# Performance work log

Hardware: AMD Instinct MI355X
Metric: run time of the kernel (lower is better)

## Reference

```python
import jax, jax.numpy as jnp
import numpy as np

D_MODEL = 1024
N_HEADS = 16
D_HEAD = D_MODEL // N_HEADS
D_FF = 4096
THETA = 10000.0
EPS = 1e-5


def rmsnorm(x, g):
    xf = x.astype(jnp.float32)
    rms = jnp.sqrt(jnp.mean(xf * xf, axis=-1, keepdims=True) + EPS)
    return ((xf / rms) * g).astype(x.dtype)


def rope(x, pos):
    # x: (B, H, S, d_head); pos: (S,) int
    dk = x.shape[-1]
    inv_freq = 1.0 / (THETA ** (jnp.arange(0, dk, 2, dtype=jnp.float32) / dk))
    freqs = pos.astype(jnp.float32)[:, None] * inv_freq[None, :]  # (S, dk/2)
    cos, sin = jnp.cos(freqs), jnp.sin(freqs)
    xp = x.reshape(*x.shape[:-1], dk // 2, 2)
    xe, xo = xp[..., 0], xp[..., 1]
    re = xe * cos - xo * sin
    ro = xe * sin + xo * cos
    return jnp.stack([re, ro], axis=-1).reshape(x.shape)


def attention(x, pos, q_w, k_w, v_w, o_w):
    B, S, D = x.shape
    def heads(t):
        return t.reshape(B, S, N_HEADS, D_HEAD).transpose(0, 2, 1, 3)
    Q = heads(x @ q_w.T)
    K = heads(x @ k_w.T)
    V = heads(x @ v_w.T)
    Q = rope(Q, pos)
    K = rope(K, pos)
    scores = jnp.einsum('bhqd,bhkd->bhqk', Q, K) / jnp.sqrt(jnp.float32(D_HEAD))
    causal = jnp.tril(jnp.ones((S, S), dtype=bool))
    scores = jnp.where(causal[None, None], scores, -jnp.inf)
    attn = jax.nn.softmax(scores, axis=-1)
    H = jnp.einsum('bhqk,bhkd->bhqd', attn, V)
    H = H.transpose(0, 2, 1, 3).reshape(B, S, D)
    return H @ o_w.T


def swiglu(x, w1, w2, w3):
    a = x @ w1.T
    swish = a * jax.nn.sigmoid(a)
    gate = x @ w3.T
    return (swish * gate) @ w2.T


def setup_inputs() -> dict:
    key = jax.random.key(0)
    ks = jax.random.split(key, 8)
    B, S = 4, 2048
    std_ff = (2.0 / (D_MODEL + D_FF)) ** 0.5
    return {
        'x': jax.random.normal(ks[0], (B, S, D_MODEL), jnp.float32),
        'token_positions': jnp.arange(S, dtype=jnp.int32),
        'q_w': jax.random.truncated_normal(ks[1], -3, 3, (D_MODEL, D_MODEL), jnp.float32),
        'k_w': jax.random.truncated_normal(ks[2], -3, 3, (D_MODEL, D_MODEL), jnp.float32),
        'v_w': jax.random.truncated_normal(ks[3], -3, 3, (D_MODEL, D_MODEL), jnp.float32),
        'o_w': jax.random.truncated_normal(ks[4], -3, 3, (D_MODEL, D_MODEL), jnp.float32),
        'g1': jnp.ones((D_MODEL,), jnp.float32),
        'g2': jnp.ones((D_MODEL,), jnp.float32),
        'w1': jax.random.truncated_normal(ks[5], -3, 3, (D_FF, D_MODEL), jnp.float32) * std_ff,
        'w2': jax.random.truncated_normal(ks[6], -3, 3, (D_MODEL, D_FF), jnp.float32) * std_ff,
        'w3': jax.random.truncated_normal(ks[7], -3, 3, (D_FF, D_MODEL), jnp.float32) * std_ff,
    }


def reference(x, token_positions, q_w, k_w, v_w, o_w, g1, g2, w1, w2, w3):
    x_norm = rmsnorm(x, g1)
    O = x + attention(x_norm, token_positions, q_w, k_w, v_w, o_w)
    H = O + swiglu(rmsnorm(O, g2), w1, w2, w3)
    return H
```

## Files before the change

### kernel.cpp

```cpp
#include <hip/hip_runtime.h>
#include <stdint.h>


typedef short bf16x8 __attribute__((ext_vector_type(8)));
typedef float f32x4  __attribute__((ext_vector_type(4)));

#define DEV static __device__ __forceinline__

DEV float bf2f(uint32_t u) { uint32_t v = u << 16; float f; __builtin_memcpy(&f, &v, 4); return f; }
DEV uint16_t f2bf(float f) {
  uint32_t u; __builtin_memcpy(&u, &f, 4);
  u = (u + 0x7fffu + ((u >> 16) & 1u)) >> 16;
  return (uint16_t)u;
}

DEV void gl_lds16(const uint16_t* g, uint16_t* l) {
  __builtin_amdgcn_global_load_lds((const __attribute__((address_space(1))) uint32_t*)g,
                                   (__attribute__((address_space(3))) uint32_t*)l, 16, 0, 0);
}


__global__ __launch_bounds__(256) void cvt_bf16_k(const float* __restrict__ src,
                                                  uint16_t* __restrict__ dst, int n4) {
  const int t = blockIdx.x * 256 + threadIdx.x;
  if (t >= n4) return;
  const float4 v = ((const float4*)src)[t];
  ushort4 o; o.x = f2bf(v.x); o.y = f2bf(v.y); o.z = f2bf(v.z); o.w = f2bf(v.w);
  ((ushort4*)dst)[t] = o;
}

__global__ __launch_bounds__(256) void cvt_split_qk_k(const float* __restrict__ qw,
                                                      const float* __restrict__ kw,
                                                      uint16_t* __restrict__ hi,
                                                      uint16_t* __restrict__ lo) {
  const int t = blockIdx.x * 256 + threadIdx.x;
  const int row = t >> 8, c4 = t & 255;
  const float* src = (row < 1024) ? (qw + (size_t)row * 1024)
                                  : (kw + (size_t)(row - 1024) * 1024);
  const float4 v = ((const float4*)src)[c4];
  ushort4 h, l;
  h.x = f2bf(v.x); l.x = f2bf(v.x - bf2f(h.x));
  h.y = f2bf(v.y); l.y = f2bf(v.y - bf2f(h.y));
  h.z = f2bf(v.z); l.z = f2bf(v.z - bf2f(h.z));
  h.w = f2bf(v.w); l.w = f2bf(v.w - bf2f(h.w));
  ((ushort4*)hi)[t] = h; ((ushort4*)lo)[t] = l;
}


template <bool SPLIT>
__global__ __launch_bounds__(256) void rmsnorm_k(const float* __restrict__ xin,
                                                 const float* __restrict__ g,
                                                 uint16_t* __restrict__ hi,
                                                 uint16_t* __restrict__ lo) {
  const int row = blockIdx.x, t = threadIdx.x;
  const float4 v = ((const float4*)(xin + (size_t)row * 1024))[t];
  float ss = v.x * v.x + v.y * v.y + v.z * v.z + v.w * v.w;
#pragma unroll
  for (int m = 1; m < 64; m <<= 1) ss += __shfl_xor(ss, m);
  __shared__ float red[4];
  if ((t & 63) == 0) red[t >> 6] = ss;
  __syncthreads();
  const float rinv = rsqrtf((red[0] + red[1] + red[2] + red[3]) * (1.0f / 1024.0f) + 1e-5f);
  const float4 gv = ((const float4*)g)[t];
  float y[4] = { v.x * rinv * gv.x, v.y * rinv * gv.y, v.z * rinv * gv.z, v.w * rinv * gv.w };
  ushort4 h; h.x = f2bf(y[0]); h.y = f2bf(y[1]); h.z = f2bf(y[2]); h.w = f2bf(y[3]);
  ((ushort4*)(hi + (size_t)row * 1024))[t] = h;
  if constexpr (SPLIT) {
    ushort4 l;
    l.x = f2bf(y[0] - bf2f(h.x)); l.y = f2bf(y[1] - bf2f(h.y));
    l.z = f2bf(y[2] - bf2f(h.z)); l.w = f2bf(y[3] - bf2f(h.w));
    ((ushort4*)(lo + (size_t)row * 1024))[t] = l;
  }
}


template <int OUT>
__global__ __launch_bounds__(256) void gemm_bt_k(const uint16_t* __restrict__ A,
                                                 const uint16_t* __restrict__ B,
                                                 void* __restrict__ C,
                                                 const float* __restrict__ resid,
                                                 int N, int K) {
  __shared__ __align__(16) uint16_t As[128 * 64];
  __shared__ __align__(16) uint16_t Bs[128 * 64];
  const int t = threadIdx.x, w = t >> 6, lane = t & 63, m16 = lane & 15, quad = lane >> 4;
  const int wm = (w >> 1) * 64, wn = (w & 1) * 64;
  const int mBase = blockIdx.y * 128, nBase = blockIdx.x * 128;
  f32x4 acc[4][4];
  const f32x4 vz = {0.f, 0.f, 0.f, 0.f};
#pragma unroll
  for (int i = 0; i < 4; ++i)
#pragma unroll
    for (int j = 0; j < 4; ++j) acc[i][j] = vz;
  const int r_ = t >> 3, g_ = t & 7, sg = g_ ^ (r_ & 7);
  const uint16_t* ag = A + (size_t)(mBase + r_) * K + sg * 8;
  const uint16_t* bg = B + (size_t)(nBase + r_) * K + sg * 8;
  for (int k0 = 0; k0 < K; k0 += 64) {
#pragma unroll
    for (int it = 0; it < 4; ++it) {
      gl_lds16(ag + (size_t)(it * 32) * K + k0, As + it * 2048 + t * 8);
      gl_lds16(bg + (size_t)(it * 32) * K + k0, Bs + it * 2048 + t * 8);
    }
    __syncthreads();
#pragma unroll
    for (int ks = 0; ks < 2; ++ks) {
      bf16x8 af[4], bf4[4];
      const int cg = ks * 4 + quad;
#pragma unroll
      for (int i = 0; i < 4; ++i) {
        const int rA = wm + i * 16 + m16;
        af[i] = *(const bf16x8*)(As + rA * 64 + ((cg ^ (rA & 7)) * 8));
        const int rB = wn + i * 16 + m16;
        bf4[i] = *(const bf16x8*)(Bs + rB * 64 + ((cg ^ (rB & 7)) * 8));
      }
#pragma unroll
      for (int i = 0; i < 4; ++i)
#pragma unroll
        for (int j = 0; j < 4; ++j)
          acc[i][j] = __builtin_amdgcn_mfma_f32_16x16x32_bf16(af[i], bf4[j], acc[i][j], 0, 0, 0);
    }
    __syncthreads();
  }
#pragma unroll
  for (int i = 0; i < 4; ++i) {
    const int row0 = mBase + wm + i * 16 + quad * 4;
#pragma unroll
    for (int j = 0; j < 4; ++j) {
      const int col = nBase + wn + j * 16 + m16;
#pragma unroll
      for (int r = 0; r < 4; ++r) {
        const size_t idx = (size_t)(row0 + r) * N + col;
        const float v = acc[i][j][r];
        if constexpr (OUT == 1) ((float*)C)[idx] = v + resid[idx];
        else                    ((uint16_t*)C)[idx] = f2bf(v);
      }
    }
  }
}


template <int OUT>
__global__ __launch_bounds__(512, 2) void gemm256_k(const uint16_t* __restrict__ A,
                                                    const uint16_t* __restrict__ B,
                                                    uint16_t* __restrict__ C,
                                                    const uint16_t* __restrict__ aux,
                                                    int N, int K) {
  __shared__ __align__(16) uint16_t As[2][256 * 64];
  __shared__ __align__(16) uint16_t Bs[2][256 * 64];
  const int t = threadIdx.x, w = t >> 6, lane = t & 63, m16 = lane & 15, quad = lane >> 4;
  const int wm = (w >> 2) * 128, wn = (w & 3) * 64;
  const int mBase = blockIdx.y * 256, nBase = blockIdx.x * 256;
  const int NT = K >> 6;

  f32x4 acc[8][4];
  const f32x4 vz = {0.f, 0.f, 0.f, 0.f};
#pragma unroll
  for (int i = 0; i < 8; ++i)
#pragma unroll
    for (int j = 0; j < 4; ++j) acc[i][j] = vz;

  const int r_ = t >> 3, g_ = t & 7, sg = g_ ^ (r_ & 7);
  const uint16_t* ag = A + (size_t)(mBase + r_) * K + sg * 8;
  const uint16_t* bg = B + (size_t)(nBase + r_) * K + sg * 8;

#define STG_A(kt, h)                                                         \
  if ((kt) < NT) {                                                           \
    uint16_t* d0 = &As[(kt) & 1][(h) * 8192 + t * 8];                        \
    const uint16_t* s0 = ag + (size_t)((h) * 128) * K + (kt) * 64;           \
    gl_lds16(s0, d0);                                                        \
    gl_lds16(s0 + (size_t)64 * K, d0 + 4096);                                \
  }
#define STG_B(kt, h)                                                         \
  if ((kt) < NT) {                                                           \
    uint16_t* d0 = &Bs[(kt) & 1][(h) * 8192 + t * 8];                        \
    const uint16_t* s0 = bg + (size_t)((h) * 128) * K + (kt) * 64;           \
    gl_lds16(s0, d0);                                                        \
    gl_lds16(s0 + (size_t)64 * K, d0 + 4096);                                \
  }

  STG_B(0, 0); STG_B(0, 1); STG_A(0, 0); STG_A(0, 1);
  STG_B(1, 0); STG_A(1, 0);

  for (int T = 0; T < NT; ++T) {
    const int c = T & 1;
    const uint16_t* Ac = As[c];
    const uint16_t* Bc = Bs[c];
    bf16x8 af[4][2], b0[2][2], b1[2][2];

    STG_B(T + 1, 1);
    if (T == NT - 1) { asm volatile("s_waitcnt vmcnt(0)" ::: "memory"); }
    else             { asm volatile("s_waitcnt vmcnt(6)" ::: "memory"); }
    __builtin_amdgcn_s_barrier();
    __builtin_amdgcn_sched_barrier(0);
#pragma unroll
    for (int i = 0; i < 4; ++i) {
      const int rA = wm + i * 16 + m16;
#pragma unroll
      for (int ks = 0; ks < 2; ++ks)
        af[i][ks] = *(const bf16x8*)(Ac + rA * 64 + (((ks * 4 + quad) ^ (rA & 7)) * 8));
    }
#pragma unroll
    for (int j = 0; j < 2; ++j) {
      const int rB = wn + j * 16 + m16;
#pragma unroll
      for (int ks = 0; ks < 2; ++ks)
        b0[j][ks] = *(const bf16x8*)(Bc + rB * 64 + (((ks * 4 + quad) ^ (rB & 7)) * 8));
    }
    __builtin_amdgcn_s_setprio(1);
#pragma unroll
    for (int ks = 0; ks < 2; ++ks)
#pragma unroll
      for (int i = 0; i < 4; ++i)
#pragma unroll
        for (int j = 0; j < 2; ++j)
          acc[i][j] = __builtin_amdgcn_mfma_f32_16x16x32_bf16(af[i][ks], b0[j][ks], acc[i][j], 0, 0, 0);
    __builtin_amdgcn_s_setprio(0);
    __builtin_amdgcn_s_barrier();

    STG_A(T + 1, 1);
#pragma unroll
    for (int j = 0; j < 2; ++j) {
      const int rB = wn + (2 + j) * 16 + m16;
#pragma unroll
      for (int ks = 0; ks < 2; ++ks)
        b1[j][ks] = *(const bf16x8*)(Bc + rB * 64 + (((ks * 4 + quad) ^ (rB & 7)) * 8));
    }
    __builtin_amdgcn_s_setprio(1);
#pragma unroll
    for (int ks = 0; ks < 2; ++ks)
#pragma unroll
      for (int i = 0; i < 4; ++i)
#pragma unroll
        for (int j = 0; j < 2; ++j)
          acc[i][2 + j] = __builtin_amdgcn_mfma_f32_16x16x32_bf16(af[i][ks], b1[j][ks], acc[i][2 + j], 0, 0, 0);
    __builtin_amdgcn_s_setprio(0);
    __builtin_amdgcn_s_barrier();

    STG_B(T + 2, 0);
#pragma unroll
    for (int i = 0; i < 4; ++i) {
      const int rA = wm + 64 + i * 16 + m16;
#pragma unroll
      for (int ks = 0; ks < 2; ++ks)
        af[i][ks] = *(const bf16x8*)(Ac + rA * 64 + (((ks * 4 + quad) ^ (rA & 7)) * 8));
    }
    __builtin_amdgcn_s_setprio(1);
#pragma unroll
    for (int ks = 0; ks < 2; ++ks)
#pragma unroll
      for (int i = 0; i < 4; ++i)
#pragma unroll
        for (int j = 0; j < 2; ++j)
          acc[4 + i][j] = __builtin_amdgcn_mfma_f32_16x16x32_bf16(af[i][ks], b0[j][ks], acc[4 + i][j], 0, 0, 0);
    __builtin_amdgcn_s_setprio(0);
    __builtin_amdgcn_s_barrier();

    STG_A(T + 2, 0);
    __builtin_amdgcn_s_setprio(1);
#pragma unroll
    for (int ks = 0; ks < 2; ++ks)
#pragma unroll
      for (int i = 0; i < 4; ++i)
#pragma unroll
        for (int j = 0; j < 2; ++j)
          acc[4 + i][2 + j] = __builtin_amdgcn_mfma_f32_16x16x32_bf16(af[i][ks], b1[j][ks], acc[4 + i][2 + j], 0, 0, 0);
    __builtin_amdgcn_s_setprio(0);
    __builtin_amdgcn_s_barrier();
  }
#undef STG_A
#undef STG_B

#pragma unroll
  for (int i = 0; i < 8; ++i) {
    const int row0 = mBase + wm + i * 16 + quad * 4;
#pragma unroll
    for (int j = 0; j < 4; ++j) {
      const int col = nBase + wn + j * 16 + m16;
#pragma unroll
      for (int r = 0; r < 4; ++r) {
        const size_t idx = (size_t)(row0 + r) * N + col;
        const float v = acc[i][j][r];
        if constexpr (OUT == 2) {
          const float a = bf2f(aux[idx]);
          const float sw = a / (1.f + __expf(-a));
          C[idx] = f2bf(sw * v);
        } else {
          C[idx] = f2bf(v);
        }
      }
    }
  }
}


__global__ __launch_bounds__(256) void gemm_bt_split_k(
    const uint16_t* __restrict__ Ahi, const uint16_t* __restrict__ Alo,
    const uint16_t* __restrict__ Bhi, const uint16_t* __restrict__ Blo,
    uint16_t* __restrict__ Chi, uint16_t* __restrict__ Clo, int N, int K) {
  __shared__ __align__(16) uint16_t Ah[128 * 32];
  __shared__ __align__(16) uint16_t Al[128 * 32];
  __shared__ __align__(16) uint16_t Bh[128 * 32];
  __shared__ __align__(16) uint16_t Bl[128 * 32];
  const int t = threadIdx.x, w = t >> 6, lane = t & 63, m16 = lane & 15, quad = lane >> 4;
  const int wm = (w >> 1) * 64, wn = (w & 1) * 64;
  const int mBase = blockIdx.y * 128, nBase = blockIdx.x * 128;
  f32x4 acc[4][4];
  const f32x4 vz = {0.f, 0.f, 0.f, 0.f};
#pragma unroll
  for (int i = 0; i < 4; ++i)
#pragma unroll
    for (int j = 0; j < 4; ++j) acc[i][j] = vz;
  const int r_ = t >> 2, g_ = t & 3, sg = g_ ^ (r_ & 3);
  const uint16_t* agh = Ahi + (size_t)(mBase + r_) * K + sg * 8;
  const uint16_t* agl = Alo + (size_t)(mBase + r_) * K + sg * 8;
  const uint16_t* bgh = Bhi + (size_t)(nBase + r_) * K + sg * 8;
  const uint16_t* bgl = Blo + (size_t)(nBase + r_) * K + sg * 8;
  for (int k0 = 0; k0 < K; k0 += 32) {
#pragma unroll
    for (int it = 0; it < 2; ++it) {
      gl_lds16(agh + (size_t)(it * 64) * K + k0, Ah + it * 2048 + t * 8);
      gl_lds16(agl + (size_t)(it * 64) * K + k0, Al + it * 2048 + t * 8);
      gl_lds16(bgh + (size_t)(it * 64) * K + k0, Bh + it * 2048 + t * 8);
      gl_lds16(bgl + (size_t)(it * 64) * K + k0, Bl + it * 2048 + t * 8);
    }
    __syncthreads();
    bf16x8 ah[4], al[4], bh4[4], bl4[4];
#pragma unroll
    for (int i = 0; i < 4; ++i) {
      const int rA = wm + i * 16 + m16;
      const int offA = rA * 32 + ((quad ^ (rA & 3)) * 8);
      ah[i] = *(const bf16x8*)(Ah + offA);
      al[i] = *(const bf16x8*)(Al + offA);
      const int rB = wn + i * 16 + m16;
      const int offB = rB * 32 + ((quad ^ (rB & 3)) * 8);
      bh4[i] = *(const bf16x8*)(Bh + offB);
      bl4[i] = *(const bf16x8*)(Bl + offB);
    }
#pragma unroll
    for (int i = 0; i < 4; ++i)
#pragma unroll
      for (int j = 0; j < 4; ++j) {
        acc[i][j] = __builtin_amdgcn_mfma_f32_16x16x32_bf16(ah[i], bh4[j], acc[i][j], 0, 0, 0);
        acc[i][j] = __builtin_amdgcn_mfma_f32_16x16x32_bf16(ah[i], bl4[j], acc[i][j], 0, 0, 0);
        acc[i][j] = __builtin_amdgcn_mfma_f32_16x16x32_bf16(al[i], bh4[j], acc[i][j], 0, 0, 0);
      }
    __syncthreads();
  }
#pragma unroll
  for (int i = 0; i < 4; ++i) {
    const int row0 = mBase + wm + i * 16 + quad * 4;
#pragma unroll
    for (int j = 0; j < 4; ++j) {
      const int col = nBase + wn + j * 16 + m16;
#pragma unroll
      for (int r = 0; r < 4; ++r) {
        const size_t idx = (size_t)(row0 + r) * N + col;
        const float v = acc[i][j][r];
        const uint16_t hh = f2bf(v);
        Chi[idx] = hh;
        Clo[idx] = f2bf(v - bf2f(hh));
      }
    }
  }
}


__global__ __launch_bounds__(256) void rope_k(uint16_t* __restrict__ qkh,
                                              uint16_t* __restrict__ qkl,
                                              const int* __restrict__ pos) {
  const int t = blockIdx.x * 256 + threadIdx.x;
  const int row = t >> 10, p = t & 1023;
  const int which = p >> 9, hp = p & 511, h = hp >> 5, d2 = hp & 31;
  const size_t idx = (size_t)row * 2048 + which * 1024 + h * 64 + d2 * 2;
  const uint32_t ph = *(const uint32_t*)(qkh + idx);
  const uint32_t pl = *(const uint32_t*)(qkl + idx);
  const float xe = bf2f(ph & 0xffffu) + bf2f(pl & 0xffffu);
  const float xo = bf2f(ph >> 16) + bf2f(pl >> 16);
  const float inv_freq = exp2f((float)d2 * -0.41524101186092029f);
  const float fr = (float)pos[row & 2047] * inv_freq;
  float sn, cs; sincosf(fr, &sn, &cs);
  const float re = xe * cs - xo * sn;
  const float ro = xe * sn + xo * cs;
  const uint16_t reh = f2bf(re), roh = f2bf(ro);
  const uint16_t rel = f2bf(re - bf2f(reh)), rol = f2bf(ro - bf2f(roh));
  *(uint32_t*)(qkh + idx) = (uint32_t)reh | ((uint32_t)roh << 16);
  *(uint32_t*)(qkl + idx) = (uint32_t)rel | ((uint32_t)rol << 16);
}


__global__ __launch_bounds__(256) void flash_k(const uint16_t* __restrict__ Qh,
                                               const uint16_t* __restrict__ Ql,
                                               const uint16_t* __restrict__ Vt,
                                               uint16_t* __restrict__ Hout) {
  __shared__ __align__(16) uint16_t Kh[2][64 * 64];
  __shared__ __align__(16) uint16_t Kl[2][64 * 64];
  __shared__ __align__(16) uint16_t Vs[2][64 * 64];
  __shared__ __align__(16) uint16_t P[4][32 * 72];

  const int bh = blockIdx.y, b = bh >> 4, h = bh & 15;
  const int t = threadIdx.x, w = t >> 6, lane = t & 63, m16 = lane & 15, quad = lane >> 4;

  const int r_ = t >> 3, g_ = t & 7, sgx = g_ ^ (r_ & 7);
  const uint16_t* khg = Qh + (size_t)(b * 2048 + r_) * 2048 + 1024 + h * 64 + sgx * 8;
  const uint16_t* klg = Ql + (size_t)(b * 2048 + r_) * 2048 + 1024 + h * 64 + sgx * 8;
  const uint16_t* vtg = Vt + (size_t)(h * 64 + r_) * 8192 + (size_t)b * 2048 + sgx * 8;

  const float nscl = 0.18033688011112042f;

  for (int half = 0; half < 2; ++half) {
    const int qt = half ? (15 - (int)blockIdx.x) : (int)blockIdx.x;

    bf16x8 qh[2][2], ql[2][2];
#pragma unroll
    for (int i = 0; i < 2; ++i) {
      const int row = b * 2048 + qt * 128 + w * 32 + i * 16 + m16;
#pragma unroll
      for (int ks = 0; ks < 2; ++ks) {
        const size_t offq = (size_t)row * 2048 + h * 64 + ks * 32 + quad * 8;
        qh[i][ks] = *(const bf16x8*)(Qh + offq);
        ql[i][ks] = *(const bf16x8*)(Ql + offq);
      }
    }
#pragma unroll
    for (int i = 0; i < 2; ++i)
#pragma unroll
      for (int ks = 0; ks < 2; ++ks)
        asm volatile("" : "+v"(qh[i][ks]), "+v"(ql[i][ks]));

    const int ktEnd = 2 * qt + 2;

#pragma unroll
    for (int it = 0; it < 2; ++it) {
      gl_lds16(khg + (size_t)(it * 32) * 2048, &Kh[0][it * 2048 + t * 8]);
      gl_lds16(klg + (size_t)(it * 32) * 2048, &Kl[0][it * 2048 + t * 8]);
      gl_lds16(vtg + (size_t)(it * 32) * 8192, &Vs[0][it * 2048 + t * 8]);
    }

    float mr[2][4], lr[2][4];
    f32x4 o[2][4];
    const f32x4 vz = {0.f, 0.f, 0.f, 0.f};
#pragma unroll
    for (int i = 0; i < 2; ++i)
#pragma unroll
      for (int r = 0; r < 4; ++r) { mr[i][r] = -1e30f; lr[i][r] = 0.f; }
#pragma unroll
    for (int i = 0; i < 2; ++i)
#pragma unroll
      for (int n = 0; n < 4; ++n) o[i][n] = vz;

    for (int kt = 0; kt < ktEnd; ++kt) {
      const int cur = kt & 1, nxt = cur ^ 1;
      __builtin_amdgcn_s_barrier();
      __builtin_amdgcn_sched_barrier(0);
      if (kt + 1 < ktEnd) {
        const int kn = kt + 1;
#pragma unroll
        for (int it = 0; it < 2; ++it) {
          gl_lds16(khg + (size_t)(kn * 64 + it * 32) * 2048, &Kh[nxt][it * 2048 + t * 8]);
          gl_lds16(klg + (size_t)(kn * 64 + it * 32) * 2048, &Kl[nxt][it * 2048 + t * 8]);
          gl_lds16(vtg + (size_t)(it * 32) * 8192 + kn * 64, &Vs[nxt][it * 2048 + t * 8]);
        }
        asm volatile("s_waitcnt vmcnt(6)" ::: "memory");
      } else {
        asm volatile("s_waitcnt vmcnt(0)" ::: "memory");
      }
      __builtin_amdgcn_s_barrier();
      __builtin_amdgcn_sched_barrier(0);

      f32x4 sc[2][4];
#pragma unroll
      for (int i = 0; i < 2; ++i)
#pragma unroll
        for (int j = 0; j < 4; ++j) sc[i][j] = vz;
#pragma unroll
      for (int ks = 0; ks < 2; ++ks) {
        bf16x8 kfh[4], kfl[4];
        const int cg = ks * 4 + quad;
#pragma unroll
        for (int j = 0; j < 4; ++j) {
          const int rK = j * 16 + m16;
          const int offk = rK * 64 + ((cg ^ (rK & 7)) * 8);
          kfh[j] = *(const bf16x8*)(&Kh[cur][offk]);
          kfl[j] = *(const bf16x8*)(&Kl[cur][offk]);
        }
        __builtin_amdgcn_s_setprio(1);
#pragma unroll
        for (int i = 0; i < 2; ++i)
#pragma unroll
          for (int j = 0; j < 4; ++j) {
            sc[i][j] = __builtin_amdgcn_mfma_f32_16x16x32_bf16(qh[i][ks], kfh[j], sc[i][j], 0, 0, 0);
            sc[i][j] = __builtin_amdgcn_mfma_f32_16x16x32_bf16(qh[i][ks], kfl[j], sc[i][j], 0, 0, 0);
            sc[i][j] = __builtin_amdgcn_mfma_f32_16x16x32_bf16(ql[i][ks], kfh[j], sc[i][j], 0, 0, 0);
          }
        __builtin_amdgcn_s_setprio(0);
      }

#pragma unroll
      for (int i = 0; i < 2; ++i) {
        const bool needMask = (kt * 64 + 63) > (qt * 128 + w * 32 + i * 16);
#pragma unroll
        for (int r = 0; r < 4; ++r) {
          float mx = -1e30f;
          if (needMask) {
            const int qg = qt * 128 + w * 32 + i * 16 + quad * 4 + r;
#pragma unroll
            for (int j = 0; j < 4; ++j) {
              float v = sc[i][j][r];
              const int kg = kt * 64 + j * 16 + m16;
              if (kg > qg) v = -1e30f;
              sc[i][j][r] = v;
              mx = fmaxf(mx, v);
            }
          } else {
#pragma unroll
            for (int j = 0; j < 4; ++j) mx = fmaxf(mx, sc[i][j][r]);
          }
#pragma unroll
          for (int m = 1; m < 16; m <<= 1) mx = fmaxf(mx, __shfl_xor(mx, m));
          const float mnew = fmaxf(mr[i][r], mx);
          const float alpha = __builtin_amdgcn_exp2f((mr[i][r] - mnew) * nscl);
          mr[i][r] = mnew;
          const float nm = mnew * nscl;
          float ls = 0.f;
#pragma unroll
          for (int j = 0; j < 4; ++j) {
            const float pv = __builtin_amdgcn_exp2f(__builtin_fmaf(sc[i][j][r], nscl, -nm));
            sc[i][j][r] = pv;
            ls += pv;
          }
#pragma unroll
          for (int m = 1; m < 16; m <<= 1) ls += __shfl_xor(ls, m);
          lr[i][r] = lr[i][r] * alpha + ls;
#pragma unroll
          for (int n = 0; n < 4; ++n) o[i][n][r] *= alpha;
        }
#pragma unroll
        for (int j = 0; j < 4; ++j)
#pragma unroll
          for (int r = 0; r < 4; ++r)
            P[w][(i * 16 + quad * 4 + r) * 72 + j * 16 + m16] = f2bf(sc[i][j][r]);
      }

#pragma unroll
      for (int ks2 = 0; ks2 < 2; ++ks2) {
        bf16x8 pf[2], vf[4];
#pragma unroll
        for (int i = 0; i < 2; ++i)
          pf[i] = *(const bf16x8*)(&P[w][(i * 16 + m16) * 72 + ks2 * 32 + quad * 8]);
        const int cg = ks2 * 4 + quad;
#pragma unroll
        for (int n = 0; n < 4; ++n) {
          const int rV = n * 16 + m16;
          vf[n] = *(const bf16x8*)(&Vs[cur][rV * 64 + ((cg ^ (rV & 7)) * 8)]);
        }
        __builtin_amdgcn_s_setprio(1);
#pragma unroll
        for (int i = 0; i < 2; ++i)
#pragma unroll
          for (int n = 0; n < 4; ++n)
            o[i][n] = __builtin_amdgcn_mfma_f32_16x16x32_bf16(pf[i], vf[n], o[i][n], 0, 0, 0);
        __builtin_amdgcn_s_setprio(0);
      }
    }

#pragma unroll
    for (int i = 0; i < 2; ++i)
#pragma unroll
      for (int r = 0; r < 4; ++r) {
        const float inv = 1.f / lr[i][r];
        const size_t row = (size_t)(b * 2048 + qt * 128 + w * 32 + i * 16 + quad * 4 + r);
#pragma unroll
        for (int n = 0; n < 4; ++n)
          Hout[row * 1024 + h * 64 + n * 16 + m16] = f2bf(o[i][n][r] * inv);
      }
    __syncthreads();
  }
}


extern "C" void kernel_launch(void* const* d_in, const int* in_sizes, int n_in,
                              void* d_out, int out_size, void* d_ws, size_t ws_size,
                              hipStream_t stream) {
  (void)in_sizes; (void)n_in; (void)out_size; (void)ws_size;
  const float* x   = (const float*)d_in[0];
  const int*   pos = (const int*)  d_in[1];
  const float* q_w = (const float*)d_in[2];
  const float* k_w = (const float*)d_in[3];
  const float* v_w = (const float*)d_in[4];
  const float* o_w = (const float*)d_in[5];
  const float* g1  = (const float*)d_in[6];
  const float* g2  = (const float*)d_in[7];
  const float* w1  = (const float*)d_in[8];
  const float* w2  = (const float*)d_in[9];
  const float* w3  = (const float*)d_in[10];

  char* ws = (char*)d_ws;
  uint16_t* wqk_hi = (uint16_t*)(ws + 0);
  uint16_t* wqk_lo = (uint16_t*)(ws + 4194304);
  uint16_t* wv     = (uint16_t*)(ws + 8388608);
  uint16_t* wo     = (uint16_t*)(ws + 10485760);
  uint16_t* w1b    = (uint16_t*)(ws + 12582912);
  uint16_t* w3b    = (uint16_t*)(ws + 20971520);
  uint16_t* w2b    = (uint16_t*)(ws + 29360128);
  uint16_t* xn_hi  = (uint16_t*)(ws + 37748736);
  uint16_t* xn_lo  = (uint16_t*)(ws + 54525952);
  uint16_t* vt     = (uint16_t*)(ws + 88080384);
  uint16_t* qk_hi  = (uint16_t*)(ws + 104857600);
  uint16_t* qk_lo  = (uint16_t*)(ws + 138412032);
  uint16_t* hbuf   = (uint16_t*)(ws + 171966464);
  float*    ores   = (float*)   (ws + 188743680);
  uint16_t* on2    = (uint16_t*)(ws + 222298112);
  uint16_t* abuf   = (uint16_t*)(ws + 104857600);
  uint16_t* gbuf   = (uint16_t*)(ws + 37748736);

  cvt_split_qk_k<<<2048, 256, 0, stream>>>(q_w, k_w, wqk_hi, wqk_lo);
  cvt_bf16_k<<<1024, 256, 0, stream>>>(v_w, wv, 262144);
  cvt_bf16_k<<<1024, 256, 0, stream>>>(o_w, wo, 262144);
  cvt_bf16_k<<<4096, 256, 0, stream>>>(w1, w1b, 1048576);
  cvt_bf16_k<<<4096, 256, 0, stream>>>(w3, w3b, 1048576);
  cvt_bf16_k<<<4096, 256, 0, stream>>>(w2, w2b, 1048576);

  rmsnorm_k<true><<<8192, 256, 0, stream>>>(x, g1, xn_hi, xn_lo);

  gemm_bt_split_k<<<dim3(16, 64), 256, 0, stream>>>(xn_hi, xn_lo, wqk_hi, wqk_lo,
                                                    qk_hi, qk_lo, 2048, 1024);
  gemm_bt_k<0><<<dim3(64, 8), 256, 0, stream>>>(wv, xn_hi, (void*)vt, nullptr, 8192, 1024);

  rope_k<<<32768, 256, 0, stream>>>(qk_hi, qk_lo, pos);

  flash_k<<<dim3(8, 64), 256, 0, stream>>>(qk_hi, qk_lo, vt, hbuf);

  gemm_bt_k<1><<<dim3(8, 64), 256, 0, stream>>>(hbuf, wo, (void*)ores, x, 1024, 1024);

  rmsnorm_k<false><<<8192, 256, 0, stream>>>(ores, g2, on2, nullptr);

  gemm256_k<0><<<dim3(16, 32), 512, 0, stream>>>(on2, w1b, abuf, nullptr, 4096, 1024);
  gemm256_k<2><<<dim3(16, 32), 512, 0, stream>>>(on2, w3b, gbuf, abuf, 4096, 1024);

  gemm_bt_k<1><<<dim3(8, 64), 256, 0, stream>>>(gbuf, w2b, d_out, ores, 1024, 4096);
}
```

Before: 807.6 us.

## Use 256x256 double-buffered split-bf16 QK GEMM and lazy softmax rescaling in flash

Replaces the 128x128 split-precision QK projection GEMM with a 256x256-tile, 512-thread kernel. It double-buffers LDS stages and interleaves the loads with four MFMA sub-phases under explicit waitcnt and barriers, to raise data reuse and overlap loads with compute. Flash attention now skips the running-max update and the rescale of the accumulator and row sum when every new row max stays within a threshold of the old max. This removes exp and multiply work per tile, at the risk of larger exponent values that the threshold is meant to bound. LDS use grows to 128KB per block for the GEMM, which limits occupancy.

```diff
diff --git a/kernel.cpp b/kernel.cpp
--- a/kernel.cpp
+++ b/kernel.cpp
@@ -292,61 +292,136 @@
 }
 
 
-__global__ __launch_bounds__(256) void gemm_bt_split_k(
+__global__ __launch_bounds__(512, 2) void gemm_split256_k(
     const uint16_t* __restrict__ Ahi, const uint16_t* __restrict__ Alo,
     const uint16_t* __restrict__ Bhi, const uint16_t* __restrict__ Blo,
     uint16_t* __restrict__ Chi, uint16_t* __restrict__ Clo, int N, int K) {
-  __shared__ __align__(16) uint16_t Ah[128 * 32];
-  __shared__ __align__(16) uint16_t Al[128 * 32];
-  __shared__ __align__(16) uint16_t Bh[128 * 32];
-  __shared__ __align__(16) uint16_t Bl[128 * 32];
+  __shared__ __align__(16) uint16_t Ah[2][256 * 32];
+  __shared__ __align__(16) uint16_t Al[2][256 * 32];
+  __shared__ __align__(16) uint16_t Bh[2][256 * 32];
+  __shared__ __align__(16) uint16_t Bl[2][256 * 32];
   const int t = threadIdx.x, w = t >> 6, lane = t & 63, m16 = lane & 15, quad = lane >> 4;
-  const int wm = (w >> 1) * 64, wn = (w & 1) * 64;
-  const int mBase = blockIdx.y * 128, nBase = blockIdx.x * 128;
-  f32x4 acc[4][4];
+  const int wm = (w >> 2) * 128, wn = (w & 3) * 64;
+  const int mBase = blockIdx.y * 256, nBase = blockIdx.x * 256;
+  const int NT = K >> 5;
+
+  f32x4 acc[8][4];
   const f32x4 vz = {0.f, 0.f, 0.f, 0.f};
 #pragma unroll
-  for (int i = 0; i < 4; ++i)
+  for (int i = 0; i < 8; ++i)
 #pragma unroll
     for (int j = 0; j < 4; ++j) acc[i][j] = vz;
+
   const int r_ = t >> 2, g_ = t & 3, sg = g_ ^ (r_ & 3);
   const uint16_t* agh = Ahi + (size_t)(mBase + r_) * K + sg * 8;
   const uint16_t* agl = Alo + (size_t)(mBase + r_) * K + sg * 8;
   const uint16_t* bgh = Bhi + (size_t)(nBase + r_) * K + sg * 8;
   const uint16_t* bgl = Blo + (size_t)(nBase + r_) * K + sg * 8;
-  for (int k0 = 0; k0 < K; k0 += 32) {
-#pragma unroll
-    for (int it = 0; it < 2; ++it) {
-      gl_lds16(agh + (size_t)(it * 64) * K + k0, Ah + it * 2048 + t * 8);
-      gl_lds16(agl + (size_t)(it * 64) * K + k0, Al + it * 2048 + t * 8);
-      gl_lds16(bgh + (size_t)(it * 64) * K + k0, Bh + it * 2048 + t * 8);
-      gl_lds16(bgl + (size_t)(it * 64) * K + k0, Bl + it * 2048 + t * 8);
-    }
-    __syncthreads();
-    bf16x8 ah[4], al[4], bh4[4], bl4[4];
+
+#define STG4(OP, base, kt)                                                   \
+  if ((kt) < NT) {                                                           \
+    uint16_t* d = &OP[(kt) & 1][t * 8];                                      \
+    const uint16_t* s = (base) + (size_t)(kt) * 32;                          \
+    gl_lds16(s, d);                                                          \
+    gl_lds16(s + (size_t)128 * K, d + 4096);                                 \
+  }
+
+  STG4(Bh, bgh, 0); STG4(Bl, bgl, 0);
+  STG4(Ah, agh, 0); STG4(Al, agl, 0);
+  STG4(Bh, bgh, 1); STG4(Bl, bgl, 1);
+
+  for (int T = 0; T < NT; ++T) {
+    const int c = T & 1;
+    bf16x8 a_h[4], a_l[4], b0h[2], b0l[2], b1h[2], b1l[2];
+
+    STG4(Ah, agh, T + 1);
+    if (T == NT - 1) { asm volatile("s_waitcnt vmcnt(0)" ::: "memory"); }
+    else             { asm volatile("s_waitcnt vmcnt(6)" ::: "memory"); }
+    __builtin_amdgcn_s_barrier();
+    __builtin_amdgcn_sched_barrier(0);
 #pragma unroll
     for (int i = 0; i < 4; ++i) {
       const int rA = wm + i * 16 + m16;
       const int offA = rA * 32 + ((quad ^ (rA & 3)) * 8);
-      ah[i] = *(const bf16x8*)(Ah + offA);
-      al[i] = *(const bf16x8*)(Al + offA);
-      const int rB = wn + i * 16 + m16;
+      a_h[i] = *(const bf16x8*)(&Ah[c][offA]);
+      a_l[i] = *(const bf16x8*)(&Al[c][offA]);
+    }
+#pragma unroll
+    for (int j = 0; j < 2; ++j) {
+      const int rB = wn + j * 16 + m16;
       const int offB = rB * 32 + ((quad ^ (rB & 3)) * 8);
-      bh4[i] = *(const bf16x8*)(Bh + offB);
-      bl4[i] = *(const bf16x8*)(Bl + offB);
-    }
+      b0h[j] = *(const bf16x8*)(&Bh[c][offB]);
+      b0l[j] = *(const bf16x8*)(&Bl[c][offB]);
+    }
+    __builtin_amdgcn_s_setprio(1);
 #pragma unroll
     for (int i = 0; i < 4; ++i)
 #pragma unroll
-      for (int j = 0; j < 4; ++j) {
-        acc[i][j] = __builtin_amdgcn_mfma_f32_16x16x32_bf16(ah[i], bh4[j], acc[i][j], 0, 0, 0);
-        acc[i][j] = __builtin_amdgcn_mfma_f32_16x16x32_bf16(ah[i], bl4[j], acc[i][j], 0, 0, 0);
-        acc[i][j] = __builtin_amdgcn_mfma_f32_16x16x32_bf16(al[i], bh4[j], acc[i][j], 0, 0, 0);
-      }
-    __syncthreads();
-  }
-#pragma unroll
-  for (int i = 0; i < 4; ++i) {
+      for (int j = 0; j < 2; ++j) {
+        acc[i][j] = __builtin_amdgcn_mfma_f32_16x16x32_bf16(a_h[i], b0h[j], acc[i][j], 0, 0, 0);
+        acc[i][j] = __builtin_amdgcn_mfma_f32_16x16x32_bf16(a_h[i], b0l[j], acc[i][j], 0, 0, 0);
+        acc[i][j] = __builtin_amdgcn_mfma_f32_16x16x32_bf16(a_l[i], b0h[j], acc[i][j], 0, 0, 0);
+      }
+    __builtin_amdgcn_s_setprio(0);
+    __builtin_amdgcn_s_barrier();
+
+    STG4(Al, agl, T + 1);
+#pragma unroll
+    for (int j = 0; j < 2; ++j) {
+      const int rB = wn + (2 + j) * 16 + m16;
+      const int offB = rB * 32 + ((quad ^ (rB & 3)) * 8);
+      b1h[j] = *(const bf16x8*)(&Bh[c][offB]);
+      b1l[j] = *(const bf16x8*)(&Bl[c][offB]);
+    }
+    __builtin_amdgcn_s_setprio(1);
+#pragma unroll
+    for (int i = 0; i < 4; ++i)
+#pragma unroll
+      for (int j = 0; j < 2; ++j) {
+        acc[i][2 + j] = __builtin_amdgcn_mfma_f32_16x16x32_bf16(a_h[i], b1h[j], acc[i][2 + j], 0, 0, 0);
+        acc[i][2 + j] = __builtin_amdgcn_mfma_f32_16x16x32_bf16(a_h[i], b1l[j], acc[i][2 + j], 0, 0, 0);
+        acc[i][2 + j] = __builtin_amdgcn_mfma_f32_16x16x32_bf16(a_l[i], b1h[j], acc[i][2 + j], 0, 0, 0);
+      }
+    __builtin_amdgcn_s_setprio(0);
+    __builtin_amdgcn_s_barrier();
+
+    STG4(Bh, bgh, T + 2);
+#pragma unroll
+    for (int i = 0; i < 4; ++i) {
+      const int rA = wm + 64 + i * 16 + m16;
+      const int offA = rA * 32 + ((quad ^ (rA & 3)) * 8);
+      a_h[i] = *(const bf16x8*)(&Ah[c][offA]);
+      a_l[i] = *(const bf16x8*)(&Al[c][offA]);
+    }
+    __builtin_amdgcn_s_setprio(1);
+#pragma unroll
+    for (int i = 0; i < 4; ++i)
+#pragma unroll
+      for (int j = 0; j < 2; ++j) {
+        acc[4 + i][j] = __builtin_amdgcn_mfma_f32_16x16x32_bf16(a_h[i], b0h[j], acc[4 + i][j], 0, 0, 0);
+        acc[4 + i][j] = __builtin_amdgcn_mfma_f32_16x16x32_bf16(a_h[i], b0l[j], acc[4 + i][j], 0, 0, 0);
+        acc[4 + i][j] = __builtin_amdgcn_mfma_f32_16x16x32_bf16(a_l[i], b0h[j], acc[4 + i][j], 0, 0, 0);
+      }
+    __builtin_amdgcn_s_setprio(0);
+    __builtin_amdgcn_s_barrier();
+
+    STG4(Bl, bgl, T + 2);
+    __builtin_amdgcn_s_setprio(1);
+#pragma unroll
+    for (int i = 0; i < 4; ++i)
+#pragma unroll
+      for (int j = 0; j < 2; ++j) {
+        acc[4 + i][2 + j] = __builtin_amdgcn_mfma_f32_16x16x32_bf16(a_h[i], b1h[j], acc[4 + i][2 + j], 0, 0, 0);
+        acc[4 + i][2 + j] = __builtin_amdgcn_mfma_f32_16x16x32_bf16(a_h[i], b1l[j], acc[4 + i][2 + j], 0, 0, 0);
+        acc[4 + i][2 + j] = __builtin_amdgcn_mfma_f32_16x16x32_bf16(a_l[i], b1h[j], acc[4 + i][2 + j], 0, 0, 0);
+      }
+    __builtin_amdgcn_s_setprio(0);
+    __builtin_amdgcn_s_barrier();
+  }
+#undef STG4
+
+#pragma unroll
+  for (int i = 0; i < 8; ++i) {
     const int row0 = mBase + wm + i * 16 + quad * 4;
 #pragma unroll
     for (int j = 0; j < 4; ++j) {
@@ -405,6 +480,7 @@
   const uint16_t* vtg = Vt + (size_t)(h * 64 + r_) * 8192 + (size_t)b * 2048 + sgx * 8;
 
   const float nscl = 0.18033688011112042f;
+  const float THRraw = 44.36f;
 
   for (int half = 0; half < 2; ++half) {
     const int qt = half ? (15 - (int)blockIdx.x) : (int)blockIdx.x;
@@ -494,12 +570,13 @@
         __builtin_amdgcn_s_setprio(0);
       }
 
+      float mx[2][4];
 #pragma unroll
       for (int i = 0; i < 2; ++i) {
         const bool needMask = (kt * 64 + 63) > (qt * 128 + w * 32 + i * 16);
 #pragma unroll
         for (int r = 0; r < 4; ++r) {
-          float mx = -1e30f;
+          float m0 = -1e30f;
           if (needMask) {
             const int qg = qt * 128 + w * 32 + i * 16 + quad * 4 + r;
 #pragma unroll
@@ -508,37 +585,71 @@
               const int kg = kt * 64 + j * 16 + m16;
               if (kg > qg) v = -1e30f;
               sc[i][j][r] = v;
-              mx = fmaxf(mx, v);
+              m0 = fmaxf(m0, v);
             }
           } else {
 #pragma unroll
-            for (int j = 0; j < 4; ++j) mx = fmaxf(mx, sc[i][j][r]);
+            for (int j = 0; j < 4; ++j) m0 = fmaxf(m0, sc[i][j][r]);
           }
 #pragma unroll
-          for (int m = 1; m < 16; m <<= 1) mx = fmaxf(mx, __shfl_xor(mx, m));
-          const float mnew = fmaxf(mr[i][r], mx);
-          const float alpha = __builtin_amdgcn_exp2f((mr[i][r] - mnew) * nscl);
-          mr[i][r] = mnew;
-          const float nm = mnew * nscl;
-          float ls = 0.f;
-#pragma unroll
-          for (int j = 0; j < 4; ++j) {
-            const float pv = __builtin_amdgcn_exp2f(__builtin_fmaf(sc[i][j][r], nscl, -nm));
-            sc[i][j][r] = pv;
-            ls += pv;
+          for (int m = 1; m < 16; m <<= 1) m0 = fmaxf(m0, __shfl_xor(m0, m));
+          mx[i][r] = m0;
+        }
+      }
+      bool allok = true;
+#pragma unroll
+      for (int i = 0; i < 2; ++i)
+#pragma unroll
+        for (int r = 0; r < 4; ++r) allok = allok && (mx[i][r] <= mr[i][r] + THRraw);
+
+      if (__all(allok)) {
+#pragma unroll
+        for (int i = 0; i < 2; ++i)
+#pragma unroll
+          for (int r = 0; r < 4; ++r) {
+            const float nm = mr[i][r] * nscl;
+            float ls = 0.f;
+#pragma unroll
+            for (int j = 0; j < 4; ++j) {
+              const float pv = __builtin_amdgcn_exp2f(__builtin_fmaf(sc[i][j][r], nscl, -nm));
+              sc[i][j][r] = pv;
+              ls += pv;
+            }
+#pragma unroll
+            for (int m = 1; m < 16; m <<= 1) ls += __shfl_xor(ls, m);
+            lr[i][r] += ls;
           }
-#pragma unroll
-          for (int m = 1; m < 16; m <<= 1) ls += __shfl_xor(ls, m);
-          lr[i][r] = lr[i][r] * alpha + ls;
-#pragma unroll
-          for (int n = 0; n < 4; ++n) o[i][n][r] *= alpha;
-        }
+      } else {
+#pragma unroll
+        for (int i = 0; i < 2; ++i)
+#pragma unroll
+          for (int r = 0; r < 4; ++r) {
+            const float mnew = fmaxf(mr[i][r], mx[i][r]);
+            const float alpha = __builtin_amdgcn_exp2f((mr[i][r] - mnew) * nscl);
+            mr[i][r] = mnew;
+            const float nm = mnew * nscl;
+            float ls = 0.f;
+#pragma unroll
+            for (int j = 0; j < 4; ++j) {
+              const float pv = __builtin_amdgcn_exp2f(__builtin_fmaf(sc[i][j][r], nscl, -nm));
+              sc[i][j][r] = pv;
+              ls += pv;
+            }
+#pragma unroll
+            for (int m = 1; m < 16; m <<= 1) ls += __shfl_xor(ls, m);
+            lr[i][r] = lr[i][r] * alpha + ls;
+#pragma unroll
+            for (int n = 0; n < 4; ++n) o[i][n][r] *= alpha;
+          }
+      }
+
+#pragma unroll
+      for (int i = 0; i < 2; ++i)
 #pragma unroll
         for (int j = 0; j < 4; ++j)
 #pragma unroll
           for (int r = 0; r < 4; ++r)
             P[w][(i * 16 + quad * 4 + r) * 72 + j * 16 + m16] = f2bf(sc[i][j][r]);
-      }
 
 #pragma unroll
       for (int ks2 = 0; ks2 < 2; ++ks2) {
@@ -621,8 +732,8 @@
 
   rmsnorm_k<true><<<8192, 256, 0, stream>>>(x, g1, xn_hi, xn_lo);
 
-  gemm_bt_split_k<<<dim3(16, 64), 256, 0, stream>>>(xn_hi, xn_lo, wqk_hi, wqk_lo,
-                                                    qk_hi, qk_lo, 2048, 1024);
+  gemm_split256_k<<<dim3(8, 32), 512, 0, stream>>>(xn_hi, xn_lo, wqk_hi, wqk_lo,
+                                                   qk_hi, qk_lo, 2048, 1024);
   gemm_bt_k<0><<<dim3(64, 8), 256, 0, stream>>>(wv, xn_hi, (void*)vt, nullptr, 8192, 1024);
 
   rope_k<<<32768, 256, 0, stream>>>(qk_hi, qk_lo, pos);
```

After: 908.2 us. 12.4% more time.
